# Kernel optimization log

Hardware: AMD Instinct MI355X
Metric: run time of the kernel (lower is better)

The kernel has to match this reference:

```python
import jax, jax.numpy as jnp
import numpy as np

N_NODES = 10000
N_EDGES = 640000
N_GRAPHS = 64
D = 128
N_BLOCKS = 2
NEG_SLOPE = 0.01  # F.leaky_relu default


def setup_inputs() -> dict:
    key = jax.random.key(0)
    ks = jax.random.split(key, 9)
    x = jax.random.normal(ks[0], (N_NODES, D), dtype=jnp.float32)
    edge_src = jax.random.randint(ks[1], (N_EDGES,), 0, N_NODES, dtype=jnp.int32)
    edge_dst = jax.random.randint(ks[2], (N_EDGES,), 0, N_NODES, dtype=jnp.int32)
    graph_ids = jnp.sort(jax.random.randint(ks[3], (N_NODES,), 0, N_GRAPHS, dtype=jnp.int32))
    s = 1.414 / np.sqrt(D)  # xavier-normal-ish scale
    Wfc = jax.random.normal(ks[4], (N_BLOCKS, D, D), dtype=jnp.float32) * s
    bfc = jnp.zeros((N_BLOCKS, D), dtype=jnp.float32)
    wl = jax.random.normal(ks[5], (N_BLOCKS, D), dtype=jnp.float32) * s
    wr = jax.random.normal(ks[6], (N_BLOCKS, D), dtype=jnp.float32) * s
    Wres = jax.random.normal(ks[7], (N_BLOCKS, D, D), dtype=jnp.float32) * s
    return {"x": x, "edge_src": edge_src, "edge_dst": edge_dst, "graph_ids": graph_ids,
            "Wfc": Wfc, "bfc": bfc, "wl": wl, "wr": wr, "Wres": Wres}


def _gat_block(x, edge_src, edge_dst, Wfc_b, bfc_b, wl_b, wr_b, Wres_b):
    # node projections: nn.Linear -> x @ W^T + b
    feat = x @ Wfc_b.T + bfc_b                       # [N, D]
    a_self = feat @ wl_b                              # [N] self_a (dst side)
    a_nb = feat @ wr_b                                # [N] attn  (src side)
    # per-edge score: leaky_relu(self_a[dst] + attn[src])
    s = a_self[edge_dst] + a_nb[edge_src]             # [E]
    s = jnp.where(s >= 0, s, NEG_SLOPE * s)
    # segment softmax over incoming edges of each dst node
    m = jax.ops.segment_max(s, edge_dst, num_segments=N_NODES)   # [N]
    e = jnp.exp(s - m[edge_dst])                                  # [E]
    denom = jax.ops.segment_sum(e, edge_dst, num_segments=N_NODES)
    w = e / denom[edge_dst]                                       # [E]
    # attention-weighted neighbor aggregation
    accum = jax.ops.segment_sum(w[:, None] * feat[edge_src], edge_dst,
                                num_segments=N_NODES)             # [N, D]
    # residual (in_size == out_size -> res_fc, no bias), then relu
    out = accum + x @ Wres_b.T
    return jax.nn.relu(out)


def reference(x, edge_src, edge_dst, graph_ids, Wfc, bfc, wl, wr, Wres):
    blocks = [
        _gat_block(x, edge_src, edge_dst, Wfc[b], bfc[b], wl[b], wr[b], Wres[b])
        for b in range(N_BLOCKS)
    ]
    h = jnp.concatenate(blocks, axis=1)               # mode='concat' -> [N, 2*D]
    # dgl.sum_nodes: per-graph sum pooling
    phis = jax.ops.segment_sum(h, graph_ids, num_segments=N_GRAPHS)  # [G, 2*D]
    return h, phis
```

## Files before the change

### kernel.cpp

```cpp
#include <hip/hip_runtime.h>
#include <hip/hip_bf16.h>
#include <math.h>

#define N_NODES 10000
#define N_EDGES 640000
#define N_GRAPHS 64
#define DIM 128
#define NEG_SLOPE 0.01f
#define NB_CSR 128
#define EDGES_PER_BLK (N_EDGES / NB_CSR)


__global__ __launch_bounds__(512) void csr_hist(const int4* __restrict__ edst4,
                                                int* __restrict__ bh) {
    __shared__ int hist[N_NODES];
    const int blk = blockIdx.x;
    const int t = threadIdx.x;
    for (int n = t; n < N_NODES; n += 512) hist[n] = 0;
    __syncthreads();
    const int base4 = blk * (EDGES_PER_BLK / 4);
    for (int i = t; i < EDGES_PER_BLK / 4; i += 512) {
        int4 d = edst4[base4 + i];
        atomicAdd(&hist[d.x], 1);
        atomicAdd(&hist[d.y], 1);
        atomicAdd(&hist[d.z], 1);
        atomicAdd(&hist[d.w], 1);
    }
    __syncthreads();
    int* dst = bh + (size_t)blk * N_NODES;
    for (int n = t; n < N_NODES; n += 512) dst[n] = hist[n];
}

__global__ __launch_bounds__(256) void csr_node_scan(int* __restrict__ bh,
                                                     int* __restrict__ deg) {
    int n = blockIdx.x * 256 + threadIdx.x;
    if (n >= N_NODES) return;
    int running = 0;
    for (int blk = 0; blk < NB_CSR; ++blk) {
        int* p = bh + (size_t)blk * N_NODES + n;
        int v = *p;
        *p = running;
        running += v;
    }
    deg[n] = running;
}

__global__ __launch_bounds__(1024) void scan_deg(const int* __restrict__ deg,
                                                 int* __restrict__ rowptr) {
    __shared__ int sdata[1024];
    const int tid = threadIdx.x;
    const int base = tid * 10;
    int cnt = N_NODES - base;
    if (cnt < 0) cnt = 0;
    if (cnt > 10) cnt = 10;
    int local[10];
    int s = 0;
    for (int i = 0; i < cnt; ++i) { local[i] = s; s += deg[base + i]; }
    sdata[tid] = s;
    __syncthreads();
    for (int off = 1; off < 1024; off <<= 1) {
        int v = 0;
        if (tid >= off) v = sdata[tid - off];
        __syncthreads();
        if (tid >= off) sdata[tid] += v;
        __syncthreads();
    }
    int pre = (tid == 0) ? 0 : sdata[tid - 1];
    for (int i = 0; i < cnt; ++i) rowptr[base + i] = pre + local[i];
    if (tid == 1023) rowptr[N_NODES] = sdata[1023];
}

__global__ __launch_bounds__(512) void csr_scatter(
    const int4* __restrict__ esrc4, const int4* __restrict__ edst4,
    const int* __restrict__ rowptr, const int* __restrict__ bh,
    int* __restrict__ csr_src) {
    __shared__ int cur[N_NODES];
    const int blk = blockIdx.x;
    const int t = threadIdx.x;
    const int* boff = bh + (size_t)blk * N_NODES;
    for (int n = t; n < N_NODES; n += 512) cur[n] = rowptr[n] + boff[n];
    __syncthreads();
    const int base4 = blk * (EDGES_PER_BLK / 4);
    for (int i = t; i < EDGES_PER_BLK / 4; i += 512) {
        int4 s = esrc4[base4 + i];
        int4 d = edst4[base4 + i];
        csr_src[atomicAdd(&cur[d.x], 1)] = s.x;
        csr_src[atomicAdd(&cur[d.y], 1)] = s.y;
        csr_src[atomicAdd(&cur[d.z], 1)] = s.z;
        csr_src[atomicAdd(&cur[d.w], 1)] = s.w;
    }
}

__device__ __forceinline__ unsigned short f2bf(float f) {
    __hip_bfloat16 h = __float2bfloat16(f);
    return *reinterpret_cast<unsigned short*>(&h);
}

__global__ __launch_bounds__(256) void gemm_xwT(
    const float* __restrict__ x, const float* __restrict__ Wfc,
    const float* __restrict__ bfc, const float* __restrict__ Wres,
    float* __restrict__ feat, float* __restrict__ resid,
    unsigned short* __restrict__ feat_b16,
    const float* __restrict__ wl, const float* __restrict__ wr,
    float* __restrict__ a_self, float* __restrict__ a_nb) {
    const int which = blockIdx.z & 1;
    const int b = blockIdx.z >> 1;
    const float* __restrict__ W = (which ? Wres : Wfc) + b * DIM * DIM;
    float* __restrict__ out = (which ? resid : feat) + (size_t)b * N_NODES * DIM;
    const int n0 = blockIdx.x * 64;
    const int j0 = blockIdx.y * 64;

    __shared__ float xs[32][68];
    __shared__ float wsh[32][68];

    const int t = threadIdx.x;
    const int tj = t & 15;
    const int tn = t >> 4;
    const int r = t >> 2;
    const int q = t & 3;

    float acc[4][4];
#pragma unroll
    for (int i = 0; i < 4; ++i)
#pragma unroll
        for (int j = 0; j < 4; ++j) acc[i][j] = 0.f;

    for (int kc = 0; kc < DIM; kc += 32) {
        {
            float v[8];
            int n = n0 + r;
            if (n < N_NODES) {
                const float* p = x + (size_t)n * DIM + kc + q * 8;
                float4 v0 = *reinterpret_cast<const float4*>(p);
                float4 v1 = *reinterpret_cast<const float4*>(p + 4);
                v[0] = v0.x; v[1] = v0.y; v[2] = v0.z; v[3] = v0.w;
                v[4] = v1.x; v[5] = v1.y; v[6] = v1.z; v[7] = v1.w;
            } else {
#pragma unroll
                for (int m = 0; m < 8; ++m) v[m] = 0.f;
            }
#pragma unroll
            for (int m = 0; m < 8; ++m) xs[q * 8 + m][r] = v[m];

            const float* pw = W + (size_t)(j0 + r) * DIM + kc + q * 8;
            float4 w0 = *reinterpret_cast<const float4*>(pw);
            float4 w1 = *reinterpret_cast<const float4*>(pw + 4);
            float wv[8] = {w0.x, w0.y, w0.z, w0.w, w1.x, w1.y, w1.z, w1.w};
#pragma unroll
            for (int m = 0; m < 8; ++m) wsh[q * 8 + m][r] = wv[m];
        }
        __syncthreads();

#pragma unroll
        for (int k = 0; k < 32; ++k) {
            float4 xv = *reinterpret_cast<const float4*>(&xs[k][4 * tn]);
            float4 wv = *reinterpret_cast<const float4*>(&wsh[k][4 * tj]);
            float xa[4] = {xv.x, xv.y, xv.z, xv.w};
            float wa[4] = {wv.x, wv.y, wv.z, wv.w};
#pragma unroll
            for (int i = 0; i < 4; ++i)
#pragma unroll
                for (int j = 0; j < 4; ++j) acc[i][j] += xa[i] * wa[j];
        }
        __syncthreads();
    }

    float wlv[4], wrv[4];
    if (!which) {
#pragma unroll
        for (int k = 0; k < 4; ++k) {
            wlv[k] = wl[b * DIM + j0 + tj * 4 + k];
            wrv[k] = wr[b * DIM + j0 + tj * 4 + k];
        }
    }

#pragma unroll
    for (int i = 0; i < 4; ++i) {
        int n = n0 + tn * 4 + i;
        int j = j0 + tj * 4;
        float4 o;
        o.x = acc[i][0]; o.y = acc[i][1]; o.z = acc[i][2]; o.w = acc[i][3];
        if (!which) {
            const float* bias = bfc + b * DIM + j;
            o.x += bias[0]; o.y += bias[1]; o.z += bias[2]; o.w += bias[3];
        }
        if (n < N_NODES) {
            *reinterpret_cast<float4*>(out + (size_t)n * DIM + j) = o;
            if (!which) {
                ushort4 u;
                u.x = f2bf(o.x); u.y = f2bf(o.y); u.z = f2bf(o.z); u.w = f2bf(o.w);
                *reinterpret_cast<ushort4*>(
                    feat_b16 + ((size_t)b * N_NODES + n) * DIM + j) = u;
            }
        }
        if (!which) {
            float ps = o.x * wlv[0] + o.y * wlv[1] + o.z * wlv[2] + o.w * wlv[3];
            float pr = o.x * wrv[0] + o.y * wrv[1] + o.z * wrv[2] + o.w * wrv[3];
#pragma unroll
            for (int off = 8; off > 0; off >>= 1) {
                ps += __shfl_xor(ps, off, 64);
                pr += __shfl_xor(pr, off, 64);
            }
            if (tj == 0 && n < N_NODES) {
                atomicAdd(&a_self[b * N_NODES + n], ps);
                atomicAdd(&a_nb[b * N_NODES + n], pr);
            }
        }
    }
}

__global__ __launch_bounds__(256) void aggregate(
    const unsigned short* __restrict__ feat_b16, const float* __restrict__ resid,
    const float* __restrict__ a_self, const float* __restrict__ a_nb,
    const int* __restrict__ rowptr, const int* __restrict__ csr_src,
    float* __restrict__ out) {
    const int wave = threadIdx.x >> 6;
    const int lane = threadIdx.x & 63;
    const int n = blockIdx.x * 4 + wave;
    const int b = blockIdx.y;
    const int q = lane >> 4;
    const int l16 = lane & 15;
    const int start = rowptr[n];
    const int end = rowptr[n + 1];

    const float* __restrict__ anb = a_nb + b * N_NODES;
    const uint4* __restrict__ fb =
        reinterpret_cast<const uint4*>(feat_b16 + (size_t)b * N_NODES * DIM);
    const float asl = a_self[b * N_NODES + n];

    float acc[8];
#pragma unroll
    for (int k = 0; k < 8; ++k) acc[k] = 0.f;
    float dpart = 0.f;

    for (int c = start; c < end; c += 64) {
        int j = c + lane;
        float e = 0.f;
        int src = 0;
        if (j < end) {
            src = csr_src[j];
            float s = asl + anb[src];
            s = (s >= 0.f) ? s : NEG_SLOPE * s;
            e = __expf(s);
        }
        dpart += e;
        int cnt = end - c;
        if (cnt > 64) cnt = 64;
        int iters = (cnt + 3) >> 2;

        float w0 = __shfl(e, q, 64);
        int s0 = __shfl(src, q, 64);
        uint4 f0 = fb[(size_t)s0 * 16 + l16];

        for (int i2 = 0; i2 < iters - 1; ++i2) {
            int idx = (i2 + 1) * 4 + q;
            float w1 = __shfl(e, idx, 64);
            int s1 = __shfl(src, idx, 64);
            uint4 f1 = fb[(size_t)s1 * 16 + l16];
#pragma unroll
            for (int k = 0; k < 4; ++k) {
                unsigned int u = (&f0.x)[k];
                float lo = __uint_as_float(u << 16);
                float hi = __uint_as_float(u & 0xffff0000u);
                acc[2 * k]     += w0 * lo;
                acc[2 * k + 1] += w0 * hi;
            }
            w0 = w1; f0 = f1;
        }
#pragma unroll
        for (int k = 0; k < 4; ++k) {
            unsigned int u = (&f0.x)[k];
            float lo = __uint_as_float(u << 16);
            float hi = __uint_as_float(u & 0xffff0000u);
            acc[2 * k]     += w0 * lo;
            acc[2 * k + 1] += w0 * hi;
        }
    }

#pragma unroll
    for (int k = 0; k < 8; ++k) {
        acc[k] += __shfl_xor(acc[k], 16, 64);
        acc[k] += __shfl_xor(acc[k], 32, 64);
    }
    float denom = dpart;
#pragma unroll
    for (int off = 32; off > 0; off >>= 1) denom += __shfl_xor(denom, off, 64);

    if (q == 0) {
        float inv = (end > start) ? 1.f / denom : 0.f;
        const float4* rr = reinterpret_cast<const float4*>(
            resid + ((size_t)b * N_NODES + n) * DIM);
        float4 r0 = rr[l16 * 2];
        float4 r1 = rr[l16 * 2 + 1];
        float4 o0, o1;
        o0.x = fmaxf(acc[0] * inv + r0.x, 0.f);
        o0.y = fmaxf(acc[1] * inv + r0.y, 0.f);
        o0.z = fmaxf(acc[2] * inv + r0.z, 0.f);
        o0.w = fmaxf(acc[3] * inv + r0.w, 0.f);
        o1.x = fmaxf(acc[4] * inv + r1.x, 0.f);
        o1.y = fmaxf(acc[5] * inv + r1.y, 0.f);
        o1.z = fmaxf(acc[6] * inv + r1.z, 0.f);
        o1.w = fmaxf(acc[7] * inv + r1.w, 0.f);
        float4* po = reinterpret_cast<float4*>(out + (size_t)n * (2 * DIM) + b * DIM);
        po[l16 * 2] = o0;
        po[l16 * 2 + 1] = o1;
    }
}

__device__ int lower_bound_dev(const int* __restrict__ a, int n, int key) {
    int lo = 0, hi = n;
    while (lo < hi) {
        int mid = (lo + hi) >> 1;
        if (a[mid] < key) lo = mid + 1;
        else hi = mid;
    }
    return lo;
}

__global__ __launch_bounds__(256) void pool_graphs(
    const float* __restrict__ h, const int* __restrict__ gids,
    float* __restrict__ phis) {
    const int g = blockIdx.x;
    const int chunk = blockIdx.y;
    const int tid = threadIdx.x;
    int lo = lower_bound_dev(gids, N_NODES, g);
    int hi = lower_bound_dev(gids, N_NODES, g + 1);
    float acc = 0.f;
    for (int n = lo + chunk; n < hi; n += 16) acc += h[(size_t)n * (2 * DIM) + tid];
    if (acc != 0.f) atomicAdd(&phis[(size_t)g * (2 * DIM) + tid], acc);
}

extern "C" void kernel_launch(void* const* d_in, const int* in_sizes, int n_in,
                              void* d_out, int out_size, void* d_ws, size_t ws_size,
                              hipStream_t stream) {
    const float* x    = (const float*)d_in[0];
    const int* esrc   = (const int*)d_in[1];
    const int* edst   = (const int*)d_in[2];
    const int* gids   = (const int*)d_in[3];
    const float* Wfc  = (const float*)d_in[4];
    const float* bfc  = (const float*)d_in[5];
    const float* wl   = (const float*)d_in[6];
    const float* wr   = (const float*)d_in[7];
    const float* Wres = (const float*)d_in[8];
    float* out = (float*)d_out;

    char* ws = (char*)d_ws;
    float* feat    = (float*)(ws + 0);
    float* resid   = (float*)(ws + 10240000);
    float* a_self  = (float*)(ws + 20480000);
    float* a_nb    = (float*)(ws + 20560000);
    int*   deg     = (int*)(ws + 20640000);
    int*   rowptr  = (int*)(ws + 20688000);
    int*   csr_src = (int*)(ws + 20784000);
    unsigned short* feat_b16 = (unsigned short*)(ws + 23344000);
    int*   bh      = (int*)(ws + 28464000);

    float* phis = out + (size_t)N_NODES * 2 * DIM;

    hipMemsetAsync(a_self, 0, 4 * N_NODES * sizeof(float), stream);
    hipMemsetAsync(phis, 0, N_GRAPHS * 2 * DIM * sizeof(float), stream);

    csr_hist<<<NB_CSR, 512, 0, stream>>>((const int4*)edst, bh);
    csr_node_scan<<<(N_NODES + 255) / 256, 256, 0, stream>>>(bh, deg);
    scan_deg<<<1, 1024, 0, stream>>>(deg, rowptr);
    csr_scatter<<<NB_CSR, 512, 0, stream>>>(
        (const int4*)esrc, (const int4*)edst, rowptr, bh, csr_src);

    gemm_xwT<<<dim3((N_NODES + 63) / 64, 2, 4), 256, 0, stream>>>(
        x, Wfc, bfc, Wres, feat, resid, feat_b16, wl, wr, a_self, a_nb);
    aggregate<<<dim3(2500, 2), 256, 0, stream>>>(
        feat_b16, resid, a_self, a_nb, rowptr, csr_src, out);
    pool_graphs<<<dim3(N_GRAPHS, 16), 256, 0, stream>>>(out, gids, phis);
}
```

Measured before the change: 168.5 us.

## Build CSR with global atomics on a side stream overlapping the GEMM

Replaces the per-block shared-memory histogram, per-node block scan and block-offset scatter with a global-atomic degree histogram and a global-atomic cursor scatter, which removes the 128x10000 block-histogram buffer and one kernel. The CSR build now runs on a second stream, forked and joined with events, so it can overlap the projection GEMM. The memset is widened to also zero deg, which sits right after a_self and a_nb. Global atomics on hot destination counters may contend, and the CSR order within each row is now nondeterministic.

Result: slower. 257.2 us (+52.6%).

```diff
diff --git a/kernel.cpp b/kernel.cpp
--- a/kernel.cpp
+++ b/kernel.cpp
@@ -7,46 +7,21 @@
 #define N_GRAPHS 64
 #define DIM 128
 #define NEG_SLOPE 0.01f
-#define NB_CSR 128
-#define EDGES_PER_BLK (N_EDGES / NB_CSR)
-
-
-__global__ __launch_bounds__(512) void csr_hist(const int4* __restrict__ edst4,
-                                                int* __restrict__ bh) {
-    __shared__ int hist[N_NODES];
-    const int blk = blockIdx.x;
-    const int t = threadIdx.x;
-    for (int n = t; n < N_NODES; n += 512) hist[n] = 0;
-    __syncthreads();
-    const int base4 = blk * (EDGES_PER_BLK / 4);
-    for (int i = t; i < EDGES_PER_BLK / 4; i += 512) {
-        int4 d = edst4[base4 + i];
-        atomicAdd(&hist[d.x], 1);
-        atomicAdd(&hist[d.y], 1);
-        atomicAdd(&hist[d.z], 1);
-        atomicAdd(&hist[d.w], 1);
-    }
-    __syncthreads();
-    int* dst = bh + (size_t)blk * N_NODES;
-    for (int n = t; n < N_NODES; n += 512) dst[n] = hist[n];
-}
-
-__global__ __launch_bounds__(256) void csr_node_scan(int* __restrict__ bh,
-                                                     int* __restrict__ deg) {
-    int n = blockIdx.x * 256 + threadIdx.x;
-    if (n >= N_NODES) return;
-    int running = 0;
-    for (int blk = 0; blk < NB_CSR; ++blk) {
-        int* p = bh + (size_t)blk * N_NODES + n;
-        int v = *p;
-        *p = running;
-        running += v;
-    }
-    deg[n] = running;
+
+
+__global__ __launch_bounds__(256) void deg_hist(const int4* __restrict__ edst4,
+                                                int* __restrict__ deg) {
+    int i = blockIdx.x * 256 + threadIdx.x;
+    int4 d = edst4[i];
+    atomicAdd(&deg[d.x], 1);
+    atomicAdd(&deg[d.y], 1);
+    atomicAdd(&deg[d.z], 1);
+    atomicAdd(&deg[d.w], 1);
 }
 
 __global__ __launch_bounds__(1024) void scan_deg(const int* __restrict__ deg,
-                                                 int* __restrict__ rowptr) {
+                                                 int* __restrict__ rowptr,
+                                                 int* __restrict__ cur) {
     __shared__ int sdata[1024];
     const int tid = threadIdx.x;
     const int base = tid * 10;
@@ -66,29 +41,24 @@
         __syncthreads();
     }
     int pre = (tid == 0) ? 0 : sdata[tid - 1];
-    for (int i = 0; i < cnt; ++i) rowptr[base + i] = pre + local[i];
+    for (int i = 0; i < cnt; ++i) {
+        int r = pre + local[i];
+        rowptr[base + i] = r;
+        cur[base + i] = r;
+    }
     if (tid == 1023) rowptr[N_NODES] = sdata[1023];
 }
 
-__global__ __launch_bounds__(512) void csr_scatter(
+__global__ __launch_bounds__(256) void csr_scatter(
     const int4* __restrict__ esrc4, const int4* __restrict__ edst4,
-    const int* __restrict__ rowptr, const int* __restrict__ bh,
-    int* __restrict__ csr_src) {
-    __shared__ int cur[N_NODES];
-    const int blk = blockIdx.x;
-    const int t = threadIdx.x;
-    const int* boff = bh + (size_t)blk * N_NODES;
-    for (int n = t; n < N_NODES; n += 512) cur[n] = rowptr[n] + boff[n];
-    __syncthreads();
-    const int base4 = blk * (EDGES_PER_BLK / 4);
-    for (int i = t; i < EDGES_PER_BLK / 4; i += 512) {
-        int4 s = esrc4[base4 + i];
-        int4 d = edst4[base4 + i];
-        csr_src[atomicAdd(&cur[d.x], 1)] = s.x;
-        csr_src[atomicAdd(&cur[d.y], 1)] = s.y;
-        csr_src[atomicAdd(&cur[d.z], 1)] = s.z;
-        csr_src[atomicAdd(&cur[d.w], 1)] = s.w;
-    }
+    int* __restrict__ cur, int* __restrict__ csr_src) {
+    int i = blockIdx.x * 256 + threadIdx.x;
+    int4 s = esrc4[i];
+    int4 d = edst4[i];
+    csr_src[atomicAdd(&cur[d.x], 1)] = s.x;
+    csr_src[atomicAdd(&cur[d.y], 1)] = s.y;
+    csr_src[atomicAdd(&cur[d.z], 1)] = s.z;
+    csr_src[atomicAdd(&cur[d.w], 1)] = s.w;
 }
 
 __device__ __forceinline__ unsigned short f2bf(float f) {
@@ -351,23 +321,36 @@
     float* a_nb    = (float*)(ws + 20560000);
     int*   deg     = (int*)(ws + 20640000);
     int*   rowptr  = (int*)(ws + 20688000);
+    int*   cur     = (int*)(ws + 20736000);
     int*   csr_src = (int*)(ws + 20784000);
     unsigned short* feat_b16 = (unsigned short*)(ws + 23344000);
-    int*   bh      = (int*)(ws + 28464000);
 
     float* phis = out + (size_t)N_NODES * 2 * DIM;
 
-    hipMemsetAsync(a_self, 0, 4 * N_NODES * sizeof(float), stream);
+    static hipStream_t s2 = nullptr;
+    static hipEvent_t evFork = nullptr, evJoin = nullptr;
+    if (s2 == nullptr) {
+        hipStreamCreateWithFlags(&s2, hipStreamNonBlocking);
+        hipEventCreateWithFlags(&evFork, hipEventDisableTiming);
+        hipEventCreateWithFlags(&evJoin, hipEventDisableTiming);
+    }
+
+    hipMemsetAsync(a_self, 0, 200000, stream);
     hipMemsetAsync(phis, 0, N_GRAPHS * 2 * DIM * sizeof(float), stream);
 
-    csr_hist<<<NB_CSR, 512, 0, stream>>>((const int4*)edst, bh);
-    csr_node_scan<<<(N_NODES + 255) / 256, 256, 0, stream>>>(bh, deg);
-    scan_deg<<<1, 1024, 0, stream>>>(deg, rowptr);
-    csr_scatter<<<NB_CSR, 512, 0, stream>>>(
-        (const int4*)esrc, (const int4*)edst, rowptr, bh, csr_src);
+    hipEventRecord(evFork, stream);
+    hipStreamWaitEvent(s2, evFork, 0);
+
+    deg_hist<<<N_EDGES / 4 / 256, 256, 0, s2>>>((const int4*)edst, deg);
+    scan_deg<<<1, 1024, 0, s2>>>(deg, rowptr, cur);
+    csr_scatter<<<N_EDGES / 4 / 256, 256, 0, s2>>>(
+        (const int4*)esrc, (const int4*)edst, cur, csr_src);
+    hipEventRecord(evJoin, s2);
 
     gemm_xwT<<<dim3((N_NODES + 63) / 64, 2, 4), 256, 0, stream>>>(
         x, Wfc, bfc, Wres, feat, resid, feat_b16, wl, wr, a_self, a_nb);
+
+    hipStreamWaitEvent(stream, evJoin, 0);
     aggregate<<<dim3(2500, 2), 256, 0, stream>>>(
         feat_b16, resid, a_self, a_nb, rowptr, csr_src, out);
     pool_graphs<<<dim3(N_GRAPHS, 16), 256, 0, stream>>>(out, gids, phis);
```

## Fuse CSR histogram into GEMM launch and tile node scan through LDS

Applied to the files above, without the earlier changes.

The CSR degree histogram now runs as an extra z-slice of the projection GEMM grid. The two independent workloads share one launch and can overlap on the GPU. The histogram packs two 16-bit counters per 32-bit LDS word, which halves its shared memory so it fits the GEMM's 20KB allocation, but it relies on per-block counts staying under 65536. The per-node scan over block histograms now stages a 128-node tile through LDS with 128-thread blocks, giving more parallel loads in flight.

After: 198.4 us. +17.7%, slower.

```diff
diff --git a/kernel.cpp b/kernel.cpp
--- a/kernel.cpp
+++ b/kernel.cpp
@@ -11,38 +11,172 @@
 #define EDGES_PER_BLK (N_EDGES / NB_CSR)
 
 
-__global__ __launch_bounds__(512) void csr_hist(const int4* __restrict__ edst4,
-                                                int* __restrict__ bh) {
-    __shared__ int hist[N_NODES];
-    const int blk = blockIdx.x;
+__device__ __forceinline__ unsigned short f2bf(float f) {
+    __hip_bfloat16 h = __float2bfloat16(f);
+    return *reinterpret_cast<unsigned short*>(&h);
+}
+
+__global__ __launch_bounds__(256) void gemm_hist(
+    const float* __restrict__ x, const float* __restrict__ Wfc,
+    const float* __restrict__ bfc, const float* __restrict__ Wres,
+    float* __restrict__ feat, float* __restrict__ resid,
+    unsigned short* __restrict__ feat_b16,
+    const float* __restrict__ wl, const float* __restrict__ wr,
+    float* __restrict__ a_self, float* __restrict__ a_nb,
+    const int4* __restrict__ edst4, int* __restrict__ bh) {
+    __shared__ __align__(16) char smem[20032];
+
+    if (blockIdx.z == 4) {
+        const int blk = blockIdx.x * 2 + blockIdx.y;
+        if (blk >= NB_CSR) return;
+        unsigned int* hist = reinterpret_cast<unsigned int*>(smem);
+        const int t = threadIdx.x;
+        for (int i = t; i < N_NODES / 2; i += 256) hist[i] = 0u;
+        __syncthreads();
+        const int base4 = blk * (EDGES_PER_BLK / 4);
+        for (int i = t; i < EDGES_PER_BLK / 4; i += 256) {
+            int4 d = edst4[base4 + i];
+            atomicAdd(&hist[d.x >> 1], 1u << ((d.x & 1) << 4));
+            atomicAdd(&hist[d.y >> 1], 1u << ((d.y & 1) << 4));
+            atomicAdd(&hist[d.z >> 1], 1u << ((d.z & 1) << 4));
+            atomicAdd(&hist[d.w >> 1], 1u << ((d.w & 1) << 4));
+        }
+        __syncthreads();
+        int* dst = bh + (size_t)blk * N_NODES;
+        for (int n = t; n < N_NODES; n += 256)
+            dst[n] = (int)((hist[n >> 1] >> ((n & 1) << 4)) & 0xffffu);
+        return;
+    }
+
+    float (*xs)[68] = reinterpret_cast<float (*)[68]>(smem);
+    float (*wsh)[68] = reinterpret_cast<float (*)[68]>(smem + 8704);
+
+    const int which = blockIdx.z & 1;
+    const int b = blockIdx.z >> 1;
+    const float* __restrict__ W = (which ? Wres : Wfc) + b * DIM * DIM;
+    float* __restrict__ out = (which ? resid : feat) + (size_t)b * N_NODES * DIM;
+    const int n0 = blockIdx.x * 64;
+    const int j0 = blockIdx.y * 64;
+
     const int t = threadIdx.x;
-    for (int n = t; n < N_NODES; n += 512) hist[n] = 0;
+    const int tj = t & 15;
+    const int tn = t >> 4;
+    const int r = t >> 2;
+    const int q = t & 3;
+
+    float acc[4][4];
+#pragma unroll
+    for (int i = 0; i < 4; ++i)
+#pragma unroll
+        for (int j = 0; j < 4; ++j) acc[i][j] = 0.f;
+
+    for (int kc = 0; kc < DIM; kc += 32) {
+        {
+            float v[8];
+            int n = n0 + r;
+            if (n < N_NODES) {
+                const float* p = x + (size_t)n * DIM + kc + q * 8;
+                float4 v0 = *reinterpret_cast<const float4*>(p);
+                float4 v1 = *reinterpret_cast<const float4*>(p + 4);
+                v[0] = v0.x; v[1] = v0.y; v[2] = v0.z; v[3] = v0.w;
+                v[4] = v1.x; v[5] = v1.y; v[6] = v1.z; v[7] = v1.w;
+            } else {
+#pragma unroll
+                for (int m = 0; m < 8; ++m) v[m] = 0.f;
+            }
+#pragma unroll
+            for (int m = 0; m < 8; ++m) xs[q * 8 + m][r] = v[m];
+
+            const float* pw = W + (size_t)(j0 + r) * DIM + kc + q * 8;
+            float4 w0 = *reinterpret_cast<const float4*>(pw);
+            float4 w1 = *reinterpret_cast<const float4*>(pw + 4);
+            float wv[8] = {w0.x, w0.y, w0.z, w0.w, w1.x, w1.y, w1.z, w1.w};
+#pragma unroll
+            for (int m = 0; m < 8; ++m) wsh[q * 8 + m][r] = wv[m];
+        }
+        __syncthreads();
+
+#pragma unroll
+        for (int k = 0; k < 32; ++k) {
+            float4 xv = *reinterpret_cast<const float4*>(&xs[k][4 * tn]);
+            float4 wv = *reinterpret_cast<const float4*>(&wsh[k][4 * tj]);
+            float xa[4] = {xv.x, xv.y, xv.z, xv.w};
+            float wa[4] = {wv.x, wv.y, wv.z, wv.w};
+#pragma unroll
+            for (int i = 0; i < 4; ++i)
+#pragma unroll
+                for (int j = 0; j < 4; ++j) acc[i][j] += xa[i] * wa[j];
+        }
+        __syncthreads();
+    }
+
+    float wlv[4], wrv[4];
+    if (!which) {
+#pragma unroll
+        for (int k = 0; k < 4; ++k) {
+            wlv[k] = wl[b * DIM + j0 + tj * 4 + k];
+            wrv[k] = wr[b * DIM + j0 + tj * 4 + k];
+        }
+    }
+
+#pragma unroll
+    for (int i = 0; i < 4; ++i) {
+        int n = n0 + tn * 4 + i;
+        int j = j0 + tj * 4;
+        float4 o;
+        o.x = acc[i][0]; o.y = acc[i][1]; o.z = acc[i][2]; o.w = acc[i][3];
+        if (!which) {
+            const float* bias = bfc + b * DIM + j;
+            o.x += bias[0]; o.y += bias[1]; o.z += bias[2]; o.w += bias[3];
+        }
+        if (n < N_NODES) {
+            *reinterpret_cast<float4*>(out + (size_t)n * DIM + j) = o;
+            if (!which) {
+                ushort4 u;
+                u.x = f2bf(o.x); u.y = f2bf(o.y); u.z = f2bf(o.z); u.w = f2bf(o.w);
+                *reinterpret_cast<ushort4*>(
+                    feat_b16 + ((size_t)b * N_NODES + n) * DIM + j) = u;
+            }
+        }
+        if (!which) {
+            float ps = o.x * wlv[0] + o.y * wlv[1] + o.z * wlv[2] + o.w * wlv[3];
+            float pr = o.x * wrv[0] + o.y * wrv[1] + o.z * wrv[2] + o.w * wrv[3];
+#pragma unroll
+            for (int off = 8; off > 0; off >>= 1) {
+                ps += __shfl_xor(ps, off, 64);
+                pr += __shfl_xor(pr, off, 64);
+            }
+            if (tj == 0 && n < N_NODES) {
+                atomicAdd(&a_self[b * N_NODES + n], ps);
+                atomicAdd(&a_nb[b * N_NODES + n], pr);
+            }
+        }
+    }
+}
+
+__global__ __launch_bounds__(128) void csr_node_scan(int* __restrict__ bh,
+                                                     int* __restrict__ deg) {
+    __shared__ int tile[NB_CSR][128];
+    const int tid = threadIdx.x;
+    const int n = blockIdx.x * 128 + tid;
+    const bool ok = (n < N_NODES);
+#pragma unroll 8
+    for (int r = 0; r < NB_CSR; ++r)
+        tile[r][tid] = ok ? bh[(size_t)r * N_NODES + n] : 0;
     __syncthreads();
-    const int base4 = blk * (EDGES_PER_BLK / 4);
-    for (int i = t; i < EDGES_PER_BLK / 4; i += 512) {
-        int4 d = edst4[base4 + i];
-        atomicAdd(&hist[d.x], 1);
-        atomicAdd(&hist[d.y], 1);
-        atomicAdd(&hist[d.z], 1);
-        atomicAdd(&hist[d.w], 1);
-    }
-    __syncthreads();
-    int* dst = bh + (size_t)blk * N_NODES;
-    for (int n = t; n < N_NODES; n += 512) dst[n] = hist[n];
-}
-
-__global__ __launch_bounds__(256) void csr_node_scan(int* __restrict__ bh,
-                                                     int* __restrict__ deg) {
-    int n = blockIdx.x * 256 + threadIdx.x;
-    if (n >= N_NODES) return;
-    int running = 0;
-    for (int blk = 0; blk < NB_CSR; ++blk) {
-        int* p = bh + (size_t)blk * N_NODES + n;
-        int v = *p;
-        *p = running;
-        running += v;
-    }
-    deg[n] = running;
+    int run = 0;
+#pragma unroll 8
+    for (int r = 0; r < NB_CSR; ++r) {
+        int v = tile[r][tid];
+        tile[r][tid] = run;
+        run += v;
+    }
+    if (ok) {
+        deg[n] = run;
+#pragma unroll 8
+        for (int r = 0; r < NB_CSR; ++r)
+            bh[(size_t)r * N_NODES + n] = tile[r][tid];
+    }
 }
 
 __global__ __launch_bounds__(1024) void scan_deg(const int* __restrict__ deg,
@@ -91,124 +225,6 @@
     }
 }
 
-__device__ __forceinline__ unsigned short f2bf(float f) {
-    __hip_bfloat16 h = __float2bfloat16(f);
-    return *reinterpret_cast<unsigned short*>(&h);
-}
-
-__global__ __launch_bounds__(256) void gemm_xwT(
-    const float* __restrict__ x, const float* __restrict__ Wfc,
-    const float* __restrict__ bfc, const float* __restrict__ Wres,
-    float* __restrict__ feat, float* __restrict__ resid,
-    unsigned short* __restrict__ feat_b16,
-    const float* __restrict__ wl, const float* __restrict__ wr,
-    float* __restrict__ a_self, float* __restrict__ a_nb) {
-    const int which = blockIdx.z & 1;
-    const int b = blockIdx.z >> 1;
-    const float* __restrict__ W = (which ? Wres : Wfc) + b * DIM * DIM;
-    float* __restrict__ out = (which ? resid : feat) + (size_t)b * N_NODES * DIM;
-    const int n0 = blockIdx.x * 64;
-    const int j0 = blockIdx.y * 64;
-
-    __shared__ float xs[32][68];
-    __shared__ float wsh[32][68];
-
-    const int t = threadIdx.x;
-    const int tj = t & 15;
-    const int tn = t >> 4;
-    const int r = t >> 2;
-    const int q = t & 3;
-
-    float acc[4][4];
-#pragma unroll
-    for (int i = 0; i < 4; ++i)
-#pragma unroll
-        for (int j = 0; j < 4; ++j) acc[i][j] = 0.f;
-
-    for (int kc = 0; kc < DIM; kc += 32) {
-        {
-            float v[8];
-            int n = n0 + r;
-            if (n < N_NODES) {
-                const float* p = x + (size_t)n * DIM + kc + q * 8;
-                float4 v0 = *reinterpret_cast<const float4*>(p);
-                float4 v1 = *reinterpret_cast<const float4*>(p + 4);
-                v[0] = v0.x; v[1] = v0.y; v[2] = v0.z; v[3] = v0.w;
-                v[4] = v1.x; v[5] = v1.y; v[6] = v1.z; v[7] = v1.w;
-            } else {
-#pragma unroll
-                for (int m = 0; m < 8; ++m) v[m] = 0.f;
-            }
-#pragma unroll
-            for (int m = 0; m < 8; ++m) xs[q * 8 + m][r] = v[m];
-
-            const float* pw = W + (size_t)(j0 + r) * DIM + kc + q * 8;
-            float4 w0 = *reinterpret_cast<const float4*>(pw);
-            float4 w1 = *reinterpret_cast<const float4*>(pw + 4);
-            float wv[8] = {w0.x, w0.y, w0.z, w0.w, w1.x, w1.y, w1.z, w1.w};
-#pragma unroll
-            for (int m = 0; m < 8; ++m) wsh[q * 8 + m][r] = wv[m];
-        }
-        __syncthreads();
-
-#pragma unroll
-        for (int k = 0; k < 32; ++k) {
-            float4 xv = *reinterpret_cast<const float4*>(&xs[k][4 * tn]);
-            float4 wv = *reinterpret_cast<const float4*>(&wsh[k][4 * tj]);
-            float xa[4] = {xv.x, xv.y, xv.z, xv.w};
-            float wa[4] = {wv.x, wv.y, wv.z, wv.w};
-#pragma unroll
-            for (int i = 0; i < 4; ++i)
-#pragma unroll
-                for (int j = 0; j < 4; ++j) acc[i][j] += xa[i] * wa[j];
-        }
-        __syncthreads();
-    }
-
-    float wlv[4], wrv[4];
-    if (!which) {
-#pragma unroll
-        for (int k = 0; k < 4; ++k) {
-            wlv[k] = wl[b * DIM + j0 + tj * 4 + k];
-            wrv[k] = wr[b * DIM + j0 + tj * 4 + k];
-        }
-    }
-
-#pragma unroll
-    for (int i = 0; i < 4; ++i) {
-        int n = n0 + tn * 4 + i;
-        int j = j0 + tj * 4;
-        float4 o;
-        o.x = acc[i][0]; o.y = acc[i][1]; o.z = acc[i][2]; o.w = acc[i][3];
-        if (!which) {
-            const float* bias = bfc + b * DIM + j;
-            o.x += bias[0]; o.y += bias[1]; o.z += bias[2]; o.w += bias[3];
-        }
-        if (n < N_NODES) {
-            *reinterpret_cast<float4*>(out + (size_t)n * DIM + j) = o;
-            if (!which) {
-                ushort4 u;
-                u.x = f2bf(o.x); u.y = f2bf(o.y); u.z = f2bf(o.z); u.w = f2bf(o.w);
-                *reinterpret_cast<ushort4*>(
-                    feat_b16 + ((size_t)b * N_NODES + n) * DIM + j) = u;
-            }
-        }
-        if (!which) {
-            float ps = o.x * wlv[0] + o.y * wlv[1] + o.z * wlv[2] + o.w * wlv[3];
-            float pr = o.x * wrv[0] + o.y * wrv[1] + o.z * wrv[2] + o.w * wrv[3];
-#pragma unroll
-            for (int off = 8; off > 0; off >>= 1) {
-                ps += __shfl_xor(ps, off, 64);
-                pr += __shfl_xor(pr, off, 64);
-            }
-            if (tj == 0 && n < N_NODES) {
-                atomicAdd(&a_self[b * N_NODES + n], ps);
-                atomicAdd(&a_nb[b * N_NODES + n], pr);
-            }
-        }
-    }
-}
-
 __global__ __launch_bounds__(256) void aggregate(
     const unsigned short* __restrict__ feat_b16, const float* __restrict__ resid,
     const float* __restrict__ a_self, const float* __restrict__ a_nb,
@@ -360,14 +376,15 @@
     hipMemsetAsync(a_self, 0, 4 * N_NODES * sizeof(float), stream);
     hipMemsetAsync(phis, 0, N_GRAPHS * 2 * DIM * sizeof(float), stream);
 
-    csr_hist<<<NB_CSR, 512, 0, stream>>>((const int4*)edst, bh);
-    csr_node_scan<<<(N_NODES + 255) / 256, 256, 0, stream>>>(bh, deg);
+    gemm_hist<<<dim3((N_NODES + 63) / 64, 2, 5), 256, 0, stream>>>(
+        x, Wfc, bfc, Wres, feat, resid, feat_b16, wl, wr, a_self, a_nb,
+        (const int4*)edst, bh);
+
+    csr_node_scan<<<(N_NODES + 127) / 128, 128, 0, stream>>>(bh, deg);
     scan_deg<<<1, 1024, 0, stream>>>(deg, rowptr);
     csr_scatter<<<NB_CSR, 512, 0, stream>>>(
         (const int4*)esrc, (const int4*)edst, rowptr, bh, csr_src);
 
-    gemm_xwT<<<dim3((N_NODES + 63) / 64, 2, 4), 256, 0, stream>>>(
-        x, Wfc, bfc, Wres, feat, resid, feat_b16, wl, wr, a_self, a_nb);
     aggregate<<<dim3(2500, 2), 256, 0, stream>>>(
         feat_b16, resid, a_self, a_nb, rowptr, csr_src, out);
     pool_graphs<<<dim3(N_GRAPHS, 16), 256, 0, stream>>>(out, gids, phis);
```

## Use bf16 MFMA for projections and precompute attention vectors algebraically

Applied to the files above, without the earlier changes.

Replaces the FP32 SIMT tiled GEMM with a bf16 MFMA kernel that converts x and W to bf16 in shared memory and stages the full K dimension at once. It stops writing the unused fp32 feat buffer. The attention scores are now computed in a separate kernel by folding wl/wr through Wfc (u = W^T w) and doing per-node dot products, which removes the atomics and the memset. The cost is bf16 rounding of the inputs, which lowers the precision of the residual and features, plus one extra small kernel launch.

After: 178.6 us. 1.06x slower.

```diff
diff --git a/kernel.cpp b/kernel.cpp
--- a/kernel.cpp
+++ b/kernel.cpp
@@ -10,6 +10,14 @@
 #define NB_CSR 128
 #define EDGES_PER_BLK (N_EDGES / NB_CSR)
 
+
+__device__ __forceinline__ unsigned short f2bf(float f) {
+    __hip_bfloat16 h = __float2bfloat16(f);
+    return *reinterpret_cast<unsigned short*>(&h);
+}
+
+typedef __attribute__((ext_vector_type(8))) short short8v;
+typedef __attribute__((ext_vector_type(4))) float f32x4;
 
 __global__ __launch_bounds__(512) void csr_hist(const int4* __restrict__ edst4,
                                                 int* __restrict__ bh) {
@@ -91,122 +99,158 @@
     }
 }
 
-__device__ __forceinline__ unsigned short f2bf(float f) {
-    __hip_bfloat16 h = __float2bfloat16(f);
-    return *reinterpret_cast<unsigned short*>(&h);
-}
-
-__global__ __launch_bounds__(256) void gemm_xwT(
+#define LDK 136
+__global__ __launch_bounds__(256) void gemm_mfma(
     const float* __restrict__ x, const float* __restrict__ Wfc,
     const float* __restrict__ bfc, const float* __restrict__ Wres,
-    float* __restrict__ feat, float* __restrict__ resid,
-    unsigned short* __restrict__ feat_b16,
+    float* __restrict__ resid, unsigned short* __restrict__ feat_b16) {
+    __shared__ unsigned short xs[64 * LDK];
+    __shared__ unsigned short wsh[128 * LDK];
+    const int which = blockIdx.y & 1;
+    const int b = blockIdx.y >> 1;
+    const float* __restrict__ W = (which ? Wres : Wfc) + (size_t)b * DIM * DIM;
+    const int n0 = blockIdx.x * 64;
+    const int t = threadIdx.x;
+
+    {
+        const int r = t >> 2;
+        const int kq = (t & 3) * 32;
+        const int n = n0 + r;
+        unsigned short tmp[32];
+        if (n < N_NODES) {
+            const float4* px = reinterpret_cast<const float4*>(x + (size_t)n * DIM + kq);
+#pragma unroll
+            for (int i = 0; i < 8; ++i) {
+                float4 v = px[i];
+                tmp[4 * i]     = f2bf(v.x);
+                tmp[4 * i + 1] = f2bf(v.y);
+                tmp[4 * i + 2] = f2bf(v.z);
+                tmp[4 * i + 3] = f2bf(v.w);
+            }
+        } else {
+#pragma unroll
+            for (int i = 0; i < 32; ++i) tmp[i] = 0;
+        }
+#pragma unroll
+        for (int i = 0; i < 4; ++i)
+            *reinterpret_cast<short8v*>(&xs[r * LDK + kq + 8 * i]) =
+                *reinterpret_cast<const short8v*>(&tmp[8 * i]);
+    }
+    {
+        const int r = t >> 1;
+        const int kh = (t & 1) * 64;
+        const float4* pw = reinterpret_cast<const float4*>(W + (size_t)r * DIM + kh);
+        unsigned short tmp[64];
+#pragma unroll
+        for (int i = 0; i < 16; ++i) {
+            float4 v = pw[i];
+            tmp[4 * i]     = f2bf(v.x);
+            tmp[4 * i + 1] = f2bf(v.y);
+            tmp[4 * i + 2] = f2bf(v.z);
+            tmp[4 * i + 3] = f2bf(v.w);
+        }
+#pragma unroll
+        for (int i = 0; i < 8; ++i)
+            *reinterpret_cast<short8v*>(&wsh[r * LDK + kh + 8 * i]) =
+                *reinterpret_cast<const short8v*>(&tmp[8 * i]);
+    }
+    __syncthreads();
+
+    const int wave = t >> 6;
+    const int lane = t & 63;
+    const int l16 = lane & 15;
+    const int l4 = lane >> 4;
+
+    f32x4 acc[8];
+#pragma unroll
+    for (int nf = 0; nf < 8; ++nf) acc[nf] = (f32x4){0.f, 0.f, 0.f, 0.f};
+
+    const int arow = wave * 16 + l16;
+#pragma unroll
+    for (int ks = 0; ks < 4; ++ks) {
+        short8v af = *reinterpret_cast<const short8v*>(
+            &xs[arow * LDK + ks * 32 + l4 * 8]);
+#pragma unroll
+        for (int nf = 0; nf < 8; ++nf) {
+            short8v bfr = *reinterpret_cast<const short8v*>(
+                &wsh[(nf * 16 + l16) * LDK + ks * 32 + l4 * 8]);
+            acc[nf] = __builtin_amdgcn_mfma_f32_16x16x32_bf16(af, bfr, acc[nf], 0, 0, 0);
+        }
+    }
+
+    const int rbase = n0 + wave * 16 + l4 * 4;
+    if (which == 0) {
+#pragma unroll
+        for (int nf = 0; nf < 8; ++nf) {
+            const float bias = bfc[b * DIM + nf * 16 + l16];
+            unsigned short* dst = feat_b16 + (size_t)b * N_NODES * DIM + nf * 16 + l16;
+#pragma unroll
+            for (int r = 0; r < 4; ++r) {
+                int n = rbase + r;
+                if (n < N_NODES) dst[(size_t)n * DIM] = f2bf(acc[nf][r] + bias);
+            }
+        }
+    } else {
+        float* dst0 = resid + (size_t)b * N_NODES * DIM;
+#pragma unroll
+        for (int nf = 0; nf < 8; ++nf) {
+#pragma unroll
+            for (int r = 0; r < 4; ++r) {
+                int n = rbase + r;
+                if (n < N_NODES) dst0[(size_t)n * DIM + nf * 16 + l16] = acc[nf][r];
+            }
+        }
+    }
+}
+
+__global__ __launch_bounds__(256) void attn_vec(
+    const float* __restrict__ x, const float* __restrict__ Wfc,
+    const float* __restrict__ bfc,
     const float* __restrict__ wl, const float* __restrict__ wr,
     float* __restrict__ a_self, float* __restrict__ a_nb) {
-    const int which = blockIdx.z & 1;
-    const int b = blockIdx.z >> 1;
-    const float* __restrict__ W = (which ? Wres : Wfc) + b * DIM * DIM;
-    float* __restrict__ out = (which ? resid : feat) + (size_t)b * N_NODES * DIM;
-    const int n0 = blockIdx.x * 64;
-    const int j0 = blockIdx.y * 64;
-
-    __shared__ float xs[32][68];
-    __shared__ float wsh[32][68];
-
+    __shared__ float u[2][2][DIM];
+    __shared__ float c[2][2];
     const int t = threadIdx.x;
-    const int tj = t & 15;
-    const int tn = t >> 4;
-    const int r = t >> 2;
-    const int q = t & 3;
-
-    float acc[4][4];
-#pragma unroll
-    for (int i = 0; i < 4; ++i)
-#pragma unroll
-        for (int j = 0; j < 4; ++j) acc[i][j] = 0.f;
-
-    for (int kc = 0; kc < DIM; kc += 32) {
-        {
-            float v[8];
-            int n = n0 + r;
-            if (n < N_NODES) {
-                const float* p = x + (size_t)n * DIM + kc + q * 8;
-                float4 v0 = *reinterpret_cast<const float4*>(p);
-                float4 v1 = *reinterpret_cast<const float4*>(p + 4);
-                v[0] = v0.x; v[1] = v0.y; v[2] = v0.z; v[3] = v0.w;
-                v[4] = v1.x; v[5] = v1.y; v[6] = v1.z; v[7] = v1.w;
-            } else {
-#pragma unroll
-                for (int m = 0; m < 8; ++m) v[m] = 0.f;
-            }
-#pragma unroll
-            for (int m = 0; m < 8; ++m) xs[q * 8 + m][r] = v[m];
-
-            const float* pw = W + (size_t)(j0 + r) * DIM + kc + q * 8;
-            float4 w0 = *reinterpret_cast<const float4*>(pw);
-            float4 w1 = *reinterpret_cast<const float4*>(pw + 4);
-            float wv[8] = {w0.x, w0.y, w0.z, w0.w, w1.x, w1.y, w1.z, w1.w};
-#pragma unroll
-            for (int m = 0; m < 8; ++m) wsh[q * 8 + m][r] = wv[m];
-        }
-        __syncthreads();
-
-#pragma unroll
-        for (int k = 0; k < 32; ++k) {
-            float4 xv = *reinterpret_cast<const float4*>(&xs[k][4 * tn]);
-            float4 wv = *reinterpret_cast<const float4*>(&wsh[k][4 * tj]);
-            float xa[4] = {xv.x, xv.y, xv.z, xv.w};
-            float wa[4] = {wv.x, wv.y, wv.z, wv.w};
-#pragma unroll
-            for (int i = 0; i < 4; ++i)
-#pragma unroll
-                for (int j = 0; j < 4; ++j) acc[i][j] += xa[i] * wa[j];
-        }
-        __syncthreads();
-    }
-
-    float wlv[4], wrv[4];
-    if (!which) {
-#pragma unroll
-        for (int k = 0; k < 4; ++k) {
-            wlv[k] = wl[b * DIM + j0 + tj * 4 + k];
-            wrv[k] = wr[b * DIM + j0 + tj * 4 + k];
-        }
-    }
-
-#pragma unroll
-    for (int i = 0; i < 4; ++i) {
-        int n = n0 + tn * 4 + i;
-        int j = j0 + tj * 4;
-        float4 o;
-        o.x = acc[i][0]; o.y = acc[i][1]; o.z = acc[i][2]; o.w = acc[i][3];
-        if (!which) {
-            const float* bias = bfc + b * DIM + j;
-            o.x += bias[0]; o.y += bias[1]; o.z += bias[2]; o.w += bias[3];
-        }
-        if (n < N_NODES) {
-            *reinterpret_cast<float4*>(out + (size_t)n * DIM + j) = o;
-            if (!which) {
-                ushort4 u;
-                u.x = f2bf(o.x); u.y = f2bf(o.y); u.z = f2bf(o.z); u.w = f2bf(o.w);
-                *reinterpret_cast<ushort4*>(
-                    feat_b16 + ((size_t)b * N_NODES + n) * DIM + j) = u;
-            }
-        }
-        if (!which) {
-            float ps = o.x * wlv[0] + o.y * wlv[1] + o.z * wlv[2] + o.w * wlv[3];
-            float pr = o.x * wrv[0] + o.y * wrv[1] + o.z * wrv[2] + o.w * wrv[3];
-#pragma unroll
-            for (int off = 8; off > 0; off >>= 1) {
-                ps += __shfl_xor(ps, off, 64);
-                pr += __shfl_xor(pr, off, 64);
-            }
-            if (tj == 0 && n < N_NODES) {
-                atomicAdd(&a_self[b * N_NODES + n], ps);
-                atomicAdd(&a_nb[b * N_NODES + n], pr);
-            }
-        }
-    }
+    for (int o = t; o < 512; o += 256) {
+        int k = o & 127;
+        int bb = (o >> 7) & 1;
+        int v = o >> 8;
+        const float* wv = (v ? wr : wl) + bb * DIM;
+        const float* Wb = Wfc + (size_t)bb * DIM * DIM;
+        float s = 0.f;
+#pragma unroll 4
+        for (int j = 0; j < DIM; ++j) s += wv[j] * Wb[j * DIM + k];
+        u[v][bb][k] = s;
+    }
+    if (t < 4) {
+        int v = t >> 1, bb = t & 1;
+        const float* wv = (v ? wr : wl) + bb * DIM;
+        const float* bias = bfc + bb * DIM;
+        float s = 0.f;
+        for (int j = 0; j < DIM; ++j) s += wv[j] * bias[j];
+        c[v][bb] = s;
+    }
+    __syncthreads();
+    int n = blockIdx.x * 256 + t;
+    if (n >= N_NODES) return;
+    const float4* px = reinterpret_cast<const float4*>(x + (size_t)n * DIM);
+    float s00 = 0.f, s01 = 0.f, s10 = 0.f, s11 = 0.f;
+#pragma unroll 8
+    for (int i = 0; i < 32; ++i) {
+        float4 v = px[i];
+        const float* u00 = &u[0][0][4 * i];
+        const float* u01 = &u[0][1][4 * i];
+        const float* u10 = &u[1][0][4 * i];
+        const float* u11 = &u[1][1][4 * i];
+        s00 += v.x * u00[0] + v.y * u00[1] + v.z * u00[2] + v.w * u00[3];
+        s01 += v.x * u01[0] + v.y * u01[1] + v.z * u01[2] + v.w * u01[3];
+        s10 += v.x * u10[0] + v.y * u10[1] + v.z * u10[2] + v.w * u10[3];
+        s11 += v.x * u11[0] + v.y * u11[1] + v.z * u11[2] + v.w * u11[3];
+    }
+    a_self[n] = s00 + c[0][0];
+    a_self[N_NODES + n] = s01 + c[0][1];
+    a_nb[n] = s10 + c[1][0];
+    a_nb[N_NODES + n] = s11 + c[1][1];
 }
 
 __global__ __launch_bounds__(256) void aggregate(
@@ -345,7 +389,6 @@
     float* out = (float*)d_out;
 
     char* ws = (char*)d_ws;
-    float* feat    = (float*)(ws + 0);
     float* resid   = (float*)(ws + 10240000);
     float* a_self  = (float*)(ws + 20480000);
     float* a_nb    = (float*)(ws + 20560000);
@@ -357,8 +400,10 @@
 
     float* phis = out + (size_t)N_NODES * 2 * DIM;
 
-    hipMemsetAsync(a_self, 0, 4 * N_NODES * sizeof(float), stream);
     hipMemsetAsync(phis, 0, N_GRAPHS * 2 * DIM * sizeof(float), stream);
+
+    attn_vec<<<(N_NODES + 255) / 256, 256, 0, stream>>>(
+        x, Wfc, bfc, wl, wr, a_self, a_nb);
 
     csr_hist<<<NB_CSR, 512, 0, stream>>>((const int4*)edst, bh);
     csr_node_scan<<<(N_NODES + 255) / 256, 256, 0, stream>>>(bh, deg);
@@ -366,8 +411,9 @@
     csr_scatter<<<NB_CSR, 512, 0, stream>>>(
         (const int4*)esrc, (const int4*)edst, rowptr, bh, csr_src);
 
-    gemm_xwT<<<dim3((N_NODES + 63) / 64, 2, 4), 256, 0, stream>>>(
-        x, Wfc, bfc, Wres, feat, resid, feat_b16, wl, wr, a_self, a_nb);
+    gemm_mfma<<<dim3((N_NODES + 63) / 64, 4), 256, 0, stream>>>(
+        x, Wfc, bfc, Wres, resid, feat_b16);
+
     aggregate<<<dim3(2500, 2), 256, 0, stream>>>(
         feat_b16, resid, a_self, a_nb, rowptr, csr_src, out);
     pool_graphs<<<dim3(N_GRAPHS, 16), 256, 0, stream>>>(out, gids, phis);
```
